# Performance work log

Hardware: AMD Instinct MI355X
Metric: run time of the kernel (lower is better)

The kernel has to match this reference:

```python
import jax, jax.numpy as jnp
import numpy as np

N = 8192
H = 512
TAU = 0.8
LAM = 0.5
EPS = 1e-8


def setup_inputs() -> dict:
    key = jax.random.key(0)
    k1, k2, k3, k4, k5 = jax.random.split(key, 5)
    xavier_std = 1.414 * np.sqrt(2.0 / (H + H))  # xavier_normal_ with gain=1.414
    return {
        "z_mp": jax.random.normal(k1, (N, H), dtype=jnp.float32),
        "z_sc": jax.random.normal(k2, (N, H), dtype=jnp.float32),
        "pos": jax.random.randint(k3, (N, N), 0, 2, dtype=jnp.int32),
        "W1": (jax.random.normal(k4, (H, H), dtype=jnp.float32) * xavier_std),
        "b1": jnp.zeros((H,), dtype=jnp.float32),
        "W2": (jax.random.normal(k5, (H, H), dtype=jnp.float32) * xavier_std),
        "b2": jnp.zeros((H,), dtype=jnp.float32),
    }


def _proj(z, W1, b1, W2, b2):
    # nn.Linear applies x @ W.T + b
    h = jax.nn.elu(z @ W1.T + b1)
    return h @ W2.T + b2


def _sim(z1, z2, tau):
    # exp(cosine_similarity / tau), computed as in the original:
    # dot(z1, z2.T) / (|z1| |z2|.T) / tau
    n1 = jnp.linalg.norm(z1, axis=-1, keepdims=True)  # [N,1]
    n2 = jnp.linalg.norm(z2, axis=-1, keepdims=True)  # [N,1]
    dot = z1 @ z2.T                                   # [N,N]
    return jnp.exp(dot / (n1 * n2.T) / tau)


def reference(z_mp, z_sc, pos, W1, b1, W2, b2):
    pos_f = pos.astype(jnp.float32)
    zp_mp = _proj(z_mp, W1, b1, W2, b2)
    zp_sc = _proj(z_sc, W1, b1, W2, b2)

    m_mp2sc = _sim(zp_mp, zp_sc, TAU)   # [N,N]
    m_sc2mp = m_mp2sc.T                 # [N,N]

    # row-normalize, masked log-mean (mp -> sc)
    s_mp = m_mp2sc / (jnp.sum(m_mp2sc, axis=1, keepdims=True) + EPS)
    lori_mp = -jnp.mean(jnp.log(jnp.sum(s_mp * pos_f, axis=-1)))

    # row-normalize, masked log-mean (sc -> mp)
    s_sc = m_sc2mp / (jnp.sum(m_sc2mp, axis=1, keepdims=True) + EPS)
    lori_sc = -jnp.mean(jnp.log(jnp.sum(s_sc * pos_f, axis=-1)))

    return LAM * lori_mp + (1.0 - LAM) * lori_sc
```

## Files before the change

### kernel.cpp

```cpp
#include <hip/hip_runtime.h>
#include <stdint.h>


#define NN 8192
#define HH 512
#define TAUF 0.8f
#define EPSF 1e-8f
#define NW (NN / 32)

typedef __attribute__((ext_vector_type(4))) float f32x4;
typedef __attribute__((ext_vector_type(2))) int i32x2;
typedef __attribute__((ext_vector_type(4))) int i32x4;
typedef __attribute__((ext_vector_type(8))) int i32x8;
typedef unsigned short u16;
typedef unsigned int u32;
typedef uint8_t u8;

typedef __attribute__((address_space(1))) void GV;
typedef __attribute__((address_space(3))) void LV;

__device__ __forceinline__ void g2l16(const void* g, void* l) {
  __builtin_amdgcn_global_load_lds((const GV*)g, (LV*)l, 16, 0, 0);
}

__device__ __forceinline__ u16 f2bf(float x) {
  u32 u = __builtin_bit_cast(u32, x);
  u = (u + 0x7fffu + ((u >> 16) & 1u)) >> 16;
  return (u16)u;
}

__device__ __forceinline__ u32 f2fp8(float x) {
  u32 u = __builtin_bit_cast(u32, x);
  u32 s = (u >> 31) << 7;
  float a = fabsf(x);
  if (a >= 0.015625f) {
    u32 b = __builtin_bit_cast(u32, a);
    b += 0x7FFFFu + ((b >> 20) & 1u);
    u32 e = (b >> 23) - 127u + 7u;
    u32 m = (b >> 20) & 7u;
    return s | (e << 3) | m;
  } else {
    int m = (int)rintf(a * 512.0f);
    return s | (u32)m;
  }
}

__device__ __forceinline__ void cast8f8(const float* __restrict__ in, u8* __restrict__ out, int i) {
  f32x4 a = *(const f32x4*)(in + i);
  f32x4 b = *(const f32x4*)(in + i + 4);
  i32x2 v;
  v.x = (int)(f2fp8(a.x) | (f2fp8(a.y) << 8) | (f2fp8(a.z) << 16) | (f2fp8(a.w) << 24));
  v.y = (int)(f2fp8(b.x) | (f2fp8(b.y) << 8) | (f2fp8(b.z) << 16) | (f2fp8(b.w) << 24));
  *(i32x2*)(out + i) = v;
}

__global__ __launch_bounds__(256)
void prep_kernel(const int* __restrict__ pos, u32* __restrict__ P,
                 const float* __restrict__ z_mp, u8* __restrict__ zbA,
                 const float* __restrict__ z_sc, u8* __restrict__ zbB,
                 const float* __restrict__ W1, u8* __restrict__ W1b,
                 const float* __restrict__ W2, u8* __restrict__ W2b) {
  int b = blockIdx.x, tid = threadIdx.x;
  if (b < 8192) {
    int gid = b * 256 + tid;
    const int* src = pos + (size_t)gid * 32;
    u32 w = 0;
#pragma unroll
    for (int c = 0; c < 8; ++c) {
      i32x4 p = *(const i32x4*)(src + c * 4);
      w |= ((u32)p.x & 1u) << (c * 4);
      w |= ((u32)p.y & 1u) << (c * 4 + 1);
      w |= ((u32)p.z & 1u) << (c * 4 + 2);
      w |= ((u32)p.w & 1u) << (c * 4 + 3);
    }
    P[gid] = w;
  } else if (b < 10240) {
    cast8f8(z_mp, zbA, ((b - 8192) * 256 + tid) * 8);
  } else if (b < 12288) {
    cast8f8(z_sc, zbB, ((b - 10240) * 256 + tid) * 8);
  } else if (b < 12416) {
    cast8f8(W1, W1b, ((b - 12288) * 256 + tid) * 8);
  } else {
    cast8f8(W2, W2b, ((b - 12416) * 256 + tid) * 8);
  }
}

template <int EPI>
__global__ __launch_bounds__(256)
void gemm_proj(const u8* __restrict__ A1, const u8* __restrict__ A2,
               const u8* __restrict__ W, const float* __restrict__ bias,
               void* __restrict__ out1, void* __restrict__ out2) {
  __shared__ __align__(16) u8 As[128 * 128];
  __shared__ __align__(16) u8 Bs[128 * 128];
  const int tid = threadIdx.x;
  const int lane = tid & 63, w = tid >> 6;
  const int lo = lane & 15, quad = lane >> 4;
  const int wy = w >> 1, wx = w & 1;
  const u8* A; char* Out; int m0;
  if (blockIdx.y < 64) { A = A1; Out = (char*)out1; m0 = blockIdx.y * 128; }
  else                 { A = A2; Out = (char*)out2; m0 = (blockIdx.y - 64) * 128; }
  const int n0 = blockIdx.x * 128;
  const int srow = lane >> 3;
  const int schunk = ((lane & 7) ^ srow) * 16;
  char* AsB = (char*)As; char* BsB = (char*)Bs;
  f32x4 acc[4][4] = {};

  for (int k0 = 0; k0 < HH; k0 += 128) {
    const u8* ga = A + (size_t)(m0 + w * 32 + srow) * HH + k0 + schunk;
    const u8* gb = W + (size_t)(n0 + w * 32 + srow) * HH + k0 + schunk;
#pragma unroll
    for (int t = 0; t < 4; ++t) {
      g2l16(ga + (size_t)(t * 8) * HH, AsB + w * 4096 + t * 1024);
      g2l16(gb + (size_t)(t * 8) * HH, BsB + w * 4096 + t * 1024);
    }
    asm volatile("s_waitcnt vmcnt(0)" ::: "memory");
    __syncthreads();
    i32x8 aF[4], bF[4];
#pragma unroll
    for (int mi = 0; mi < 4; ++mi) {
      int ar = wy * 64 + mi * 16 + lo;
      int sw = ar & 7;
      i32x4 p0 = *(const i32x4*)(AsB + ar * 128 + ((2 * quad) ^ sw) * 16);
      i32x4 p1 = *(const i32x4*)(AsB + ar * 128 + ((2 * quad + 1) ^ sw) * 16);
      aF[mi] = __builtin_shufflevector(p0, p1, 0, 1, 2, 3, 4, 5, 6, 7);
    }
#pragma unroll
    for (int ni = 0; ni < 4; ++ni) {
      int br = wx * 64 + ni * 16 + lo;
      int sw = br & 7;
      i32x4 p0 = *(const i32x4*)(BsB + br * 128 + ((2 * quad) ^ sw) * 16);
      i32x4 p1 = *(const i32x4*)(BsB + br * 128 + ((2 * quad + 1) ^ sw) * 16);
      bF[ni] = __builtin_shufflevector(p0, p1, 0, 1, 2, 3, 4, 5, 6, 7);
    }
#pragma unroll
    for (int mi = 0; mi < 4; ++mi)
#pragma unroll
      for (int ni = 0; ni < 4; ++ni)
        acc[mi][ni] = __builtin_amdgcn_mfma_scale_f32_16x16x128_f8f6f4(
            aF[mi], bF[ni], acc[mi][ni], 0, 0, 0, 127, 0, 127);
    __syncthreads();
  }
#pragma unroll
  for (int mi = 0; mi < 4; ++mi) {
    int rl = wy * 64 + mi * 16 + quad * 4;
#pragma unroll
    for (int ni = 0; ni < 4; ++ni) {
      int cl = wx * 64 + ni * 16 + lo;
      float bv = bias[n0 + cl];
#pragma unroll
      for (int r = 0; r < 4; ++r) {
        float v = acc[mi][ni][r] + bv;
        size_t idx = (size_t)(m0 + rl + r) * HH + (n0 + cl);
        if (EPI == 0) {
          if (v < 0.f) v = __expf(v) - 1.f;
          ((u8*)Out)[idx] = (u8)f2fp8(v);
        } else {
          ((float*)Out)[idx] = v;
        }
      }
    }
  }
}

__global__ void norm_kernel(const float* __restrict__ zpA, u8* __restrict__ znA,
                            const float* __restrict__ zpB, u8* __restrict__ znB) {
  const int row = blockIdx.x & (NN - 1);
  const bool isA = blockIdx.x < NN;
  const float* src = (isA ? zpA : zpB) + (size_t)row * HH;
  u8* dst = (isA ? znA : znB) + (size_t)row * HH;
  const float scale = isA ? (1.0f / TAUF) : 1.0f;
  const int t = threadIdx.x;
  f32x4 v = *(const f32x4*)(src + t * 4);
  float ss = v.x * v.x + v.y * v.y + v.z * v.z + v.w * v.w;
#pragma unroll
  for (int d = 1; d < 64; d <<= 1) ss += __shfl_xor(ss, d, 64);
  __shared__ float red[2];
  if ((t & 63) == 0) red[t >> 6] = ss;
  __syncthreads();
  float inv = scale * rsqrtf(red[0] + red[1]);
  u32 o = f2fp8(v.x * inv) | (f2fp8(v.y * inv) << 8) |
          (f2fp8(v.z * inv) << 16) | (f2fp8(v.w * inv) << 24);
  *(u32*)(dst + t * 4) = o;
}

__global__ __launch_bounds__(256)
void sim_kernel(const u8* __restrict__ Az, const u8* __restrict__ Bz,
                const u32* __restrict__ Pbits,
                float* __restrict__ rowpart, float* __restrict__ posrowpart,
                float* __restrict__ colpart, float* __restrict__ poscolpart) {
  __shared__ __align__(16) u8 As[128 * 128];
  __shared__ __align__(16) u8 Bs[128 * 128];
  __shared__ u32 PBi[128 * 4];
  __shared__ u32 PBj[128 * 4];
  const int tid = threadIdx.x;
  const int lane = tid & 63, w = tid >> 6;
  const int lo = lane & 15, quad = lane >> 4;
  const int wy = w >> 1, wx = w & 1;

  const int bid = blockIdx.x + (int)gridDim.x * blockIdx.y;
  const int xcd = bid & 7, s = bid >> 3;
  const int by = xcd * 8 + (s >> 6);
  const int bx = s & 63;
  const int i0 = by * 128, j0 = bx * 128;

  const int il = tid >> 1, w2 = (tid & 1) * 2;
  const u32* PiSrc = Pbits + (size_t)(i0 + il) * NW + (j0 >> 5) + w2;
  const u32* PjSrc = Pbits + (size_t)(j0 + il) * NW + (i0 >> 5) + w2;
  u32 pa0 = PiSrc[0], pa1 = PiSrc[1], pb0 = PjSrc[0], pb1 = PjSrc[1];

  const int srow = lane >> 3;
  const int schunk = ((lane & 7) ^ srow) * 16;
  char* AsB = (char*)As; char* BsB = (char*)Bs;
  f32x4 acc[4][4] = {};

  for (int k0 = 0; k0 < HH; k0 += 128) {
    const u8* ga = Az + (size_t)(i0 + w * 32 + srow) * HH + k0 + schunk;
    const u8* gb = Bz + (size_t)(j0 + w * 32 + srow) * HH + k0 + schunk;
#pragma unroll
    for (int t = 0; t < 4; ++t) {
      g2l16(ga + (size_t)(t * 8) * HH, AsB + w * 4096 + t * 1024);
      g2l16(gb + (size_t)(t * 8) * HH, BsB + w * 4096 + t * 1024);
    }
    asm volatile("s_waitcnt vmcnt(0)" ::: "memory");
    __syncthreads();
    i32x8 aF[4], bF[4];
#pragma unroll
    for (int mi = 0; mi < 4; ++mi) {
      int ar = wy * 64 + mi * 16 + lo;
      int sw = ar & 7;
      i32x4 p0 = *(const i32x4*)(AsB + ar * 128 + ((2 * quad) ^ sw) * 16);
      i32x4 p1 = *(const i32x4*)(AsB + ar * 128 + ((2 * quad + 1) ^ sw) * 16);
      aF[mi] = __builtin_shufflevector(p0, p1, 0, 1, 2, 3, 4, 5, 6, 7);
    }
#pragma unroll
    for (int ni = 0; ni < 4; ++ni) {
      int br = wx * 64 + ni * 16 + lo;
      int sw = br & 7;
      i32x4 p0 = *(const i32x4*)(BsB + br * 128 + ((2 * quad) ^ sw) * 16);
      i32x4 p1 = *(const i32x4*)(BsB + br * 128 + ((2 * quad + 1) ^ sw) * 16);
      bF[ni] = __builtin_shufflevector(p0, p1, 0, 1, 2, 3, 4, 5, 6, 7);
    }
#pragma unroll
    for (int mi = 0; mi < 4; ++mi)
#pragma unroll
      for (int ni = 0; ni < 4; ++ni)
        acc[mi][ni] = __builtin_amdgcn_mfma_scale_f32_16x16x128_f8f6f4(
            aF[mi], bF[ni], acc[mi][ni], 0, 0, 0, 127, 0, 127);
    __syncthreads();
  }

  PBi[il * 4 + w2] = pa0; PBi[il * 4 + w2 + 1] = pa1;
  PBj[il * 4 + w2] = pb0; PBj[il * 4 + w2 + 1] = pb1;

#pragma unroll
  for (int mi = 0; mi < 4; ++mi)
#pragma unroll
    for (int ni = 0; ni < 4; ++ni)
#pragma unroll
      for (int r = 0; r < 4; ++r)
        acc[mi][ni][r] = __expf(acc[mi][ni][r]);

  __syncthreads();

  const int rowb = wy * 64 + quad * 4;
  const int colb = wx * 64 + lo;

#pragma unroll
  for (int mi = 0; mi < 4; ++mi) {
    int rl = rowb + mi * 16;
    float rs[4], pr[4];
#pragma unroll
    for (int r = 0; r < 4; ++r) {
      u32 W0 = PBi[(rl + r) * 4 + wx * 2];
      u32 W1 = PBi[(rl + r) * 4 + wx * 2 + 1];
      float e0 = acc[mi][0][r], e1 = acc[mi][1][r];
      float e2 = acc[mi][2][r], e3 = acc[mi][3][r];
      rs[r] = (e0 + e1) + (e2 + e3);
      pr[r] = (((W0 >> lo) & 1u) ? e0 : 0.f) + (((W0 >> (16 + lo)) & 1u) ? e1 : 0.f) +
              (((W1 >> lo) & 1u) ? e2 : 0.f) + (((W1 >> (16 + lo)) & 1u) ? e3 : 0.f);
    }
#pragma unroll
    for (int d = 1; d < 16; d <<= 1) {
#pragma unroll
      for (int r = 0; r < 4; ++r) {
        rs[r] += __shfl_xor(rs[r], d, 64);
        pr[r] += __shfl_xor(pr[r], d, 64);
      }
    }
    if (lo == 0) {
      float* rp = rowpart + (size_t)(bx * 2 + wx) * NN;
      float* pp = posrowpart + (size_t)(bx * 2 + wx) * NN;
#pragma unroll
      for (int r = 0; r < 4; ++r) {
        rp[i0 + rl + r] = rs[r];
        pp[i0 + rl + r] = pr[r];
      }
    }
  }

#pragma unroll
  for (int ni = 0; ni < 4; ++ni) {
    int cl = colb + ni * 16;
    u32 W0 = PBj[cl * 4 + wy * 2];
    u32 W1 = PBj[cl * 4 + wy * 2 + 1];
    float cs = 0.f, pc = 0.f;
#pragma unroll
    for (int mi = 0; mi < 4; ++mi) {
      u32 W = (mi < 2) ? W0 : W1;
      int sh = (mi & 1) * 16 + quad * 4;
#pragma unroll
      for (int r = 0; r < 4; ++r) {
        float e = acc[mi][ni][r];
        cs += e;
        pc += ((W >> (sh + r)) & 1u) ? e : 0.f;
      }
    }
    cs += __shfl_xor(cs, 16, 64); cs += __shfl_xor(cs, 32, 64);
    pc += __shfl_xor(pc, 16, 64); pc += __shfl_xor(pc, 32, 64);
    if (quad == 0) {
      colpart[(size_t)(by * 2 + wy) * NN + j0 + cl] = cs;
      poscolpart[(size_t)(by * 2 + wy) * NN + j0 + cl] = pc;
    }
  }
}

__global__ __launch_bounds__(256)
void reduce1_kernel(const float* __restrict__ rowpart, const float* __restrict__ posrowpart,
                    const float* __restrict__ colpart, const float* __restrict__ poscolpart,
                    float* __restrict__ red) {
  int t = threadIdx.x;
  int i = blockIdx.x * 128 + (t >> 1);
  int half = t & 1;
  float rs = 0.f, pr = 0.f, cs = 0.f, pc = 0.f;
  for (int s = half * 64; s < half * 64 + 64; ++s) {
    rs += rowpart[(size_t)s * NN + i];
    pr += posrowpart[(size_t)s * NN + i];
    cs += colpart[(size_t)s * NN + i];
    pc += poscolpart[(size_t)s * NN + i];
  }
  rs += __shfl_xor(rs, 1, 64); pr += __shfl_xor(pr, 1, 64);
  cs += __shfl_xor(cs, 1, 64); pc += __shfl_xor(pc, 1, 64);
  float term = (half == 0) ? (__logf(pr / (rs + EPSF)) + __logf(pc / (cs + EPSF))) : 0.f;
#pragma unroll
  for (int d = 2; d < 64; d <<= 1) term += __shfl_xor(term, d, 64);
  __shared__ float rsh[4];
  if ((t & 63) == 0) rsh[t >> 6] = term;
  __syncthreads();
  if (t == 0) red[blockIdx.x] = rsh[0] + rsh[1] + rsh[2] + rsh[3];
}

__global__ void reduce2_kernel(const float* __restrict__ red, float* __restrict__ out) {
  float s = red[threadIdx.x];
#pragma unroll
  for (int d = 1; d < 64; d <<= 1) s += __shfl_xor(s, d, 64);
  if (threadIdx.x == 0) out[0] = -0.5f * s / (float)NN;
}

extern "C" void kernel_launch(void* const* d_in, const int* in_sizes, int n_in,
                              void* d_out, int out_size, void* d_ws, size_t ws_size,
                              hipStream_t stream) {
  const float* z_mp = (const float*)d_in[0];
  const float* z_sc = (const float*)d_in[1];
  const int* pos = (const int*)d_in[2];
  const float* W1 = (const float*)d_in[3];
  const float* b1 = (const float*)d_in[4];
  const float* W2 = (const float*)d_in[5];
  const float* b2 = (const float*)d_in[6];
  float* out = (float*)d_out;

  char* ws = (char*)d_ws;
  u32* Pbits = (u32*)(ws);
  u8* zbA = (u8*)(ws + 8388608);
  u8* zbB = (u8*)(ws + 16777216);
  u8* W1b = (u8*)(ws + 25165824);
  u8* W2b = (u8*)(ws + 25690112);
  u8* hA  = (u8*)(ws + 26214400);
  u8* hB  = (u8*)(ws + 34603008);
  float* zpA = (float*)(ws + 42991616);
  float* zpB = (float*)(ws + 59768832);
  u8* znA = zbA;
  u8* znB = zbB;
  float* rowpart    = (float*)(ws + 26214400);
  float* posrowpart = (float*)(ws + 30408704);
  float* colpart    = (float*)(ws + 34603008);
  float* poscolpart = (float*)(ws + 38797312);
  float* red64 = (float*)(ws + 76546048);

  prep_kernel<<<12544, 256, 0, stream>>>(pos, Pbits, z_mp, zbA, z_sc, zbB, W1, W1b, W2, W2b);

  dim3 gp(4, 128);
  gemm_proj<0><<<gp, 256, 0, stream>>>(zbA, zbB, W1b, b1, hA, hB);
  gemm_proj<1><<<gp, 256, 0, stream>>>(hA, hB, W2b, b2, zpA, zpB);

  norm_kernel<<<2 * NN, 128, 0, stream>>>(zpA, znA, zpB, znB);

  dim3 gs(64, 64);
  sim_kernel<<<gs, 256, 0, stream>>>(znA, znB, Pbits, rowpart, posrowpart, colpart, poscolpart);
  reduce1_kernel<<<64, 256, 0, stream>>>(rowpart, posrowpart, colpart, poscolpart, red64);
  reduce2_kernel<<<1, 64, 0, stream>>>(red64, out);
}
```

Before: 525.3 us.

## Give each wave private LDS tiles to drop block barriers in GEMM loops

Each wave now stages its own 64-row A and B slices into a private LDS region, so the K loop needs no block-wide barriers. The next K chunk's loads are issued right after the current fragments are read into registers, overlapping global-to-LDS traffic with the MFMAs. The cost is duplicated global loads, since waves sharing a row or column fetch the same data, and LDS use grows to 64KB per block, which may lower occupancy.

```diff
diff --git a/kernel.cpp b/kernel.cpp
--- a/kernel.cpp
+++ b/kernel.cpp
@@ -21,12 +21,6 @@
 
 __device__ __forceinline__ void g2l16(const void* g, void* l) {
   __builtin_amdgcn_global_load_lds((const GV*)g, (LV*)l, 16, 0, 0);
-}
-
-__device__ __forceinline__ u16 f2bf(float x) {
-  u32 u = __builtin_bit_cast(u32, x);
-  u = (u + 0x7fffu + ((u >> 16) & 1u)) >> 16;
-  return (u16)u;
 }
 
 __device__ __forceinline__ u32 f2fp8(float x) {
@@ -90,8 +84,7 @@
 void gemm_proj(const u8* __restrict__ A1, const u8* __restrict__ A2,
                const u8* __restrict__ W, const float* __restrict__ bias,
                void* __restrict__ out1, void* __restrict__ out2) {
-  __shared__ __align__(16) u8 As[128 * 128];
-  __shared__ __align__(16) u8 Bs[128 * 128];
+  __shared__ __align__(16) u8 LB[4][16384];
   const int tid = threadIdx.x;
   const int lane = tid & 63, w = tid >> 6;
   const int lo = lane & 15, quad = lane >> 4;
@@ -100,37 +93,42 @@
   if (blockIdx.y < 64) { A = A1; Out = (char*)out1; m0 = blockIdx.y * 128; }
   else                 { A = A2; Out = (char*)out2; m0 = (blockIdx.y - 64) * 128; }
   const int n0 = blockIdx.x * 128;
-  const int srow = lane >> 3;
-  const int schunk = ((lane & 7) ^ srow) * 16;
-  char* AsB = (char*)As; char* BsB = (char*)Bs;
+
+  const int srow8 = lane >> 3;
+  const int schunk = ((lane & 7) ^ srow8) * 16;
+  char* lA = (char*)LB[w];
+  char* lB = lA + 8192;
+  const u8* gA = A + (size_t)(m0 + wy * 64 + srow8) * HH + schunk;
+  const u8* gB = W + (size_t)(n0 + wx * 64 + srow8) * HH + schunk;
+
+#pragma unroll
+  for (int t = 0; t < 8; ++t) {
+    g2l16(gA + (size_t)(t * 8) * HH, lA + t * 1024);
+    g2l16(gB + (size_t)(t * 8) * HH, lB + t * 1024);
+  }
   f32x4 acc[4][4] = {};
-
-  for (int k0 = 0; k0 < HH; k0 += 128) {
-    const u8* ga = A + (size_t)(m0 + w * 32 + srow) * HH + k0 + schunk;
-    const u8* gb = W + (size_t)(n0 + w * 32 + srow) * HH + k0 + schunk;
-#pragma unroll
-    for (int t = 0; t < 4; ++t) {
-      g2l16(ga + (size_t)(t * 8) * HH, AsB + w * 4096 + t * 1024);
-      g2l16(gb + (size_t)(t * 8) * HH, BsB + w * 4096 + t * 1024);
-    }
+  for (int kq = 0; kq < 4; ++kq) {
     asm volatile("s_waitcnt vmcnt(0)" ::: "memory");
-    __syncthreads();
     i32x8 aF[4], bF[4];
 #pragma unroll
     for (int mi = 0; mi < 4; ++mi) {
-      int ar = wy * 64 + mi * 16 + lo;
-      int sw = ar & 7;
-      i32x4 p0 = *(const i32x4*)(AsB + ar * 128 + ((2 * quad) ^ sw) * 16);
-      i32x4 p1 = *(const i32x4*)(AsB + ar * 128 + ((2 * quad + 1) ^ sw) * 16);
+      int ar = mi * 16 + lo, sw = ar & 7;
+      i32x4 p0 = *(const i32x4*)(lA + ar * 128 + ((2 * quad) ^ sw) * 16);
+      i32x4 p1 = *(const i32x4*)(lA + ar * 128 + ((2 * quad + 1) ^ sw) * 16);
       aF[mi] = __builtin_shufflevector(p0, p1, 0, 1, 2, 3, 4, 5, 6, 7);
-    }
-#pragma unroll
-    for (int ni = 0; ni < 4; ++ni) {
-      int br = wx * 64 + ni * 16 + lo;
-      int sw = br & 7;
-      i32x4 p0 = *(const i32x4*)(BsB + br * 128 + ((2 * quad) ^ sw) * 16);
-      i32x4 p1 = *(const i32x4*)(BsB + br * 128 + ((2 * quad + 1) ^ sw) * 16);
-      bF[ni] = __builtin_shufflevector(p0, p1, 0, 1, 2, 3, 4, 5, 6, 7);
+      i32x4 q0 = *(const i32x4*)(lB + ar * 128 + ((2 * quad) ^ sw) * 16);
+      i32x4 q1 = *(const i32x4*)(lB + ar * 128 + ((2 * quad + 1) ^ sw) * 16);
+      bF[mi] = __builtin_shufflevector(q0, q1, 0, 1, 2, 3, 4, 5, 6, 7);
+    }
+    asm volatile("s_waitcnt lgkmcnt(0)" ::: "memory");
+    if (kq < 3) {
+      const u8* gA2 = gA + (kq + 1) * 128;
+      const u8* gB2 = gB + (kq + 1) * 128;
+#pragma unroll
+      for (int t = 0; t < 8; ++t) {
+        g2l16(gA2 + (size_t)(t * 8) * HH, lA + t * 1024);
+        g2l16(gB2 + (size_t)(t * 8) * HH, lB + t * 1024);
+      }
     }
 #pragma unroll
     for (int mi = 0; mi < 4; ++mi)
@@ -138,7 +136,6 @@
       for (int ni = 0; ni < 4; ++ni)
         acc[mi][ni] = __builtin_amdgcn_mfma_scale_f32_16x16x128_f8f6f4(
             aF[mi], bF[ni], acc[mi][ni], 0, 0, 0, 127, 0, 127);
-    __syncthreads();
   }
 #pragma unroll
   for (int mi = 0; mi < 4; ++mi) {
@@ -188,10 +185,9 @@
                 const u32* __restrict__ Pbits,
                 float* __restrict__ rowpart, float* __restrict__ posrowpart,
                 float* __restrict__ colpart, float* __restrict__ poscolpart) {
-  __shared__ __align__(16) u8 As[128 * 128];
-  __shared__ __align__(16) u8 Bs[128 * 128];
-  __shared__ u32 PBi[128 * 4];
-  __shared__ u32 PBj[128 * 4];
+  __shared__ __align__(16) u8 LB[4][16384];
+  u32* PBi = (u32*)&LB[0][0];
+  u32* PBj = (u32*)&LB[0][2048];
   const int tid = threadIdx.x;
   const int lane = tid & 63, w = tid >> 6;
   const int lo = lane & 15, quad = lane >> 4;
@@ -208,37 +204,41 @@
   const u32* PjSrc = Pbits + (size_t)(j0 + il) * NW + (i0 >> 5) + w2;
   u32 pa0 = PiSrc[0], pa1 = PiSrc[1], pb0 = PjSrc[0], pb1 = PjSrc[1];
 
-  const int srow = lane >> 3;
-  const int schunk = ((lane & 7) ^ srow) * 16;
-  char* AsB = (char*)As; char* BsB = (char*)Bs;
+  const int srow8 = lane >> 3;
+  const int schunk = ((lane & 7) ^ srow8) * 16;
+  char* lA = (char*)LB[w];
+  char* lB = lA + 8192;
+  const u8* gA = Az + (size_t)(i0 + wy * 64 + srow8) * HH + schunk;
+  const u8* gB = Bz + (size_t)(j0 + wx * 64 + srow8) * HH + schunk;
+
+#pragma unroll
+  for (int t = 0; t < 8; ++t) {
+    g2l16(gA + (size_t)(t * 8) * HH, lA + t * 1024);
+    g2l16(gB + (size_t)(t * 8) * HH, lB + t * 1024);
+  }
   f32x4 acc[4][4] = {};
-
-  for (int k0 = 0; k0 < HH; k0 += 128) {
-    const u8* ga = Az + (size_t)(i0 + w * 32 + srow) * HH + k0 + schunk;
-    const u8* gb = Bz + (size_t)(j0 + w * 32 + srow) * HH + k0 + schunk;
-#pragma unroll
-    for (int t = 0; t < 4; ++t) {
-      g2l16(ga + (size_t)(t * 8) * HH, AsB + w * 4096 + t * 1024);
-      g2l16(gb + (size_t)(t * 8) * HH, BsB + w * 4096 + t * 1024);
-    }
+  for (int kq = 0; kq < 4; ++kq) {
     asm volatile("s_waitcnt vmcnt(0)" ::: "memory");
-    __syncthreads();
     i32x8 aF[4], bF[4];
 #pragma unroll
     for (int mi = 0; mi < 4; ++mi) {
-      int ar = wy * 64 + mi * 16 + lo;
-      int sw = ar & 7;
-      i32x4 p0 = *(const i32x4*)(AsB + ar * 128 + ((2 * quad) ^ sw) * 16);
-      i32x4 p1 = *(const i32x4*)(AsB + ar * 128 + ((2 * quad + 1) ^ sw) * 16);
+      int ar = mi * 16 + lo, sw = ar & 7;
+      i32x4 p0 = *(const i32x4*)(lA + ar * 128 + ((2 * quad) ^ sw) * 16);
+      i32x4 p1 = *(const i32x4*)(lA + ar * 128 + ((2 * quad + 1) ^ sw) * 16);
       aF[mi] = __builtin_shufflevector(p0, p1, 0, 1, 2, 3, 4, 5, 6, 7);
-    }
-#pragma unroll
-    for (int ni = 0; ni < 4; ++ni) {
-      int br = wx * 64 + ni * 16 + lo;
-      int sw = br & 7;
-      i32x4 p0 = *(const i32x4*)(BsB + br * 128 + ((2 * quad) ^ sw) * 16);
-      i32x4 p1 = *(const i32x4*)(BsB + br * 128 + ((2 * quad + 1) ^ sw) * 16);
-      bF[ni] = __builtin_shufflevector(p0, p1, 0, 1, 2, 3, 4, 5, 6, 7);
+      i32x4 q0 = *(const i32x4*)(lB + ar * 128 + ((2 * quad) ^ sw) * 16);
+      i32x4 q1 = *(const i32x4*)(lB + ar * 128 + ((2 * quad + 1) ^ sw) * 16);
+      bF[mi] = __builtin_shufflevector(q0, q1, 0, 1, 2, 3, 4, 5, 6, 7);
+    }
+    asm volatile("s_waitcnt lgkmcnt(0)" ::: "memory");
+    if (kq < 3) {
+      const u8* gA2 = gA + (kq + 1) * 128;
+      const u8* gB2 = gB + (kq + 1) * 128;
+#pragma unroll
+      for (int t = 0; t < 8; ++t) {
+        g2l16(gA2 + (size_t)(t * 8) * HH, lA + t * 1024);
+        g2l16(gB2 + (size_t)(t * 8) * HH, lB + t * 1024);
+      }
     }
 #pragma unroll
     for (int mi = 0; mi < 4; ++mi)
@@ -246,9 +246,9 @@
       for (int ni = 0; ni < 4; ++ni)
         acc[mi][ni] = __builtin_amdgcn_mfma_scale_f32_16x16x128_f8f6f4(
             aF[mi], bF[ni], acc[mi][ni], 0, 0, 0, 127, 0, 127);
-    __syncthreads();
-  }
-
+  }
+
+  __syncthreads();
   PBi[il * 4 + w2] = pa0; PBi[il * 4 + w2 + 1] = pa1;
   PBj[il * 4 + w2] = pb0; PBj[il * 4 + w2 + 1] = pb1;
 
```

Result: no change. 534.7 us (+1.8%).
